# Performance work log

Hardware: AMD Instinct MI355X
Metric: run time of the kernel (lower is better)

## Reference

```python
import jax, jax.numpy as jnp
import numpy as np

B, S, DIM = 2, 1024, 1024
N_EXPERTS, K = 8, 2
VOCAB = 16384
HIDDEN = DIM * 8 // 3          # 2730
UP_OUT = HIDDEN * 2            # 5460 (swiglu doubling)


def setup_inputs() -> dict:
    key = jax.random.key(0)
    ks = jax.random.split(key, 5)
    x = jax.random.normal(ks[0], (B, S, DIM), dtype=jnp.float32)
    w_router = jax.random.normal(ks[1], (N_EXPERTS, DIM), dtype=jnp.float32) * 0.02
    w_up = jax.random.normal(ks[2], (N_EXPERTS, UP_OUT, DIM), dtype=jnp.float32) * 0.02
    w_down = jax.random.normal(ks[3], (N_EXPERTS, DIM, HIDDEN), dtype=jnp.float32) * 0.02
    w_proj = jax.random.normal(ks[4], (N_EXPERTS, VOCAB, DIM), dtype=jnp.float32) * 0.02
    return {"x": x, "w_router": w_router, "w_up": w_up, "w_down": w_down, "w_proj": w_proj}


def _grouped_linear(x_sorted, weight, group_sizes):
    # weight: [n_experts, out, in] (torch Linear layout) -> ragged_dot wants [g, in, out]
    return jax.lax.ragged_dot(x_sorted, jnp.swapaxes(weight, 1, 2), group_sizes)


def reference(x, w_router, w_up, w_down, w_proj):
    b, s, d = x.shape
    # Router (eval path): plain top-k of linear scores
    scores = jnp.einsum("bsd,nd->bsn", x, w_router)
    c, ids = jax.lax.top_k(scores, K)                   # [B,S,K]
    # Dispatch: replicate tokens k times, sort by expert id (stable, matching torch.sort)
    xe = jnp.broadcast_to(x[..., None, :], (b, s, K, d)).reshape(-1, d)   # [T, d]
    ids_flat = ids.reshape(-1)
    order = jnp.argsort(ids_flat)                        # stable sort indices
    x_sorted = xe[order]
    group_sizes = jnp.bincount(ids_flat, length=N_EXPERTS).astype(jnp.int32)
    # Expert swiglu MLP with residual (grouped GEMMs)
    skip = x_sorted
    h = _grouped_linear(x_sorted, w_up, group_sizes)     # [T, 2*HIDDEN]
    h_lin, h_gate = jnp.split(h, 2, axis=-1)
    h = h_lin * jax.nn.silu(h_gate)
    h = _grouped_linear(h, w_down, group_sizes) + skip   # [T, d]
    logits = _grouped_linear(h, w_proj, group_sizes)     # [T, VOCAB]
    # Postprocess: scatter back to original token order
    out = jnp.zeros_like(logits).at[order].set(logits)
    out = out.reshape(b, s, K, VOCAB)
    # Weighted top-k combine
    w = jax.nn.softmax(c, axis=-1)                       # [B,S,K]
    return jnp.sum(out * w[..., None], axis=-2)          # [B,S,VOCAB]
```

## Files before the change

kernel.cpp:

```cpp
#include <hip/hip_runtime.h>
#include <hip/hip_bf16.h>

typedef __bf16 bf16_t;
typedef __bf16 bf16x2 __attribute__((ext_vector_type(2)));
typedef __bf16 bf16x4 __attribute__((ext_vector_type(4)));
typedef __bf16 bf16x8 __attribute__((ext_vector_type(8)));
typedef float f32x4 __attribute__((ext_vector_type(4)));

#define DIM     1024
#define NEXP    8
#define VOCAB   16384
#define HIDDEN  2730
#define UPOUT   5460
#define NTOK    2048
#define NSLOT   4096
#define HRAW_LD 5472
#define H1_LD   2752
#define BM      256
#define MAXTILES 24

#define WS_COUNTS      0
#define WS_NTILES      64
#define WS_TILE_E      128
#define WS_TILE_M0     256
#define WS_TILE_MEND   384
#define WS_SLOT_IDS    1024
#define WS_SLOT_W      20480
#define WS_SLOT_OF_POS 40960
#define WS_POS_OF_SLOT 61440
#define WS_XSORTED     131072
#define WS_H2          8519680
#define WS_H1          16908288
#define WS_HRAW        39452672
#define WS_LOGITS      16908288ull
#define WS_NEED_BIG    (WS_LOGITS + (size_t)NSLOT * VOCAB * 2)

__device__ __forceinline__ void gload_lds16(const void* g, void* l) {
    __builtin_amdgcn_global_load_lds((const __attribute__((address_space(1))) void*)g,
                                     (__attribute__((address_space(3))) void*)l, 16, 0, 0);
}
__device__ __forceinline__ int swzm(int r) { return (r ^ (r >> 2)) & 3; }

__global__ __launch_bounds__(256) void router_kernel(const float* __restrict__ x,
        const float* __restrict__ wr, int* __restrict__ slot_ids,
        float* __restrict__ slot_w, int* __restrict__ counts) {
    const int lane = threadIdx.x & 63;
    const int wave = threadIdx.x >> 6;
    const int token = blockIdx.x * 4 + wave;
    const float* xrow = x + (size_t)token * DIM;
    float acc[NEXP];
#pragma unroll
    for (int e = 0; e < NEXP; ++e) acc[e] = 0.f;
#pragma unroll
    for (int i = 0; i < DIM / 64; ++i) {
        const int k = i * 64 + lane;
        const float xv = xrow[k];
#pragma unroll
        for (int e = 0; e < NEXP; ++e) acc[e] += xv * wr[e * DIM + k];
    }
#pragma unroll
    for (int off = 32; off > 0; off >>= 1) {
#pragma unroll
        for (int e = 0; e < NEXP; ++e) acc[e] += __shfl_xor(acc[e], off);
    }
    if (lane == 0) {
        float c0 = -1e30f; int b0 = 0;
#pragma unroll
        for (int e = 0; e < NEXP; ++e) if (acc[e] > c0) { c0 = acc[e]; b0 = e; }
        float c1 = -1e30f; int b1 = 0;
#pragma unroll
        for (int e = 0; e < NEXP; ++e) if (e != b0 && acc[e] > c1) { c1 = acc[e]; b1 = e; }
        slot_ids[token * 2 + 0] = b0;
        slot_ids[token * 2 + 1] = b1;
        const float w0 = 1.f / (1.f + expf(c1 - c0));
        slot_w[token * 2 + 0] = w0;
        slot_w[token * 2 + 1] = 1.f - w0;
        atomicAdd(&counts[b0], 1);
        atomicAdd(&counts[b1], 1);
    }
}

__global__ __launch_bounds__(512) void sched_kernel(const int* __restrict__ counts,
        int* __restrict__ ntiles, int* __restrict__ tile_e, int* __restrict__ tile_m0,
        int* __restrict__ tile_mend, const int* __restrict__ slot_ids,
        int* __restrict__ slot_of_pos, int* __restrict__ pos_of_slot) {
    __shared__ int offs[NEXP];
    if (threadIdx.x == 0) {
        int o = 0, nt = 0;
        for (int e = 0; e < NEXP; ++e) {
            offs[e] = o;
            const int c = counts[e];
            for (int m = 0; m < c; m += BM) {
                tile_e[nt] = e; tile_m0[nt] = o + m; tile_mend[nt] = o + c; ++nt;
            }
            o += c;
        }
        *ntiles = nt;
    }
    __syncthreads();
    const int e = threadIdx.x >> 6;
    const int lane = threadIdx.x & 63;
    int base = offs[e];
    for (int ch = 0; ch < NSLOT / 64; ++ch) {
        const int i = ch * 64 + lane;
        const int id = slot_ids[i];
        const unsigned long long m = __ballot(id == e);
        if (id == e) {
            const int rank = __popcll(m & ((1ull << lane) - 1ull));
            slot_of_pos[base + rank] = i;
            pos_of_slot[i] = base + rank;
        }
        base += __popcll(m);
    }
}

__global__ __launch_bounds__(256) void gather_kernel(const float* __restrict__ x,
        const int* __restrict__ slot_of_pos, bf16_t* __restrict__ xs) {
    const int row = blockIdx.x;
    const int t = threadIdx.x;
    const int tok = slot_of_pos[row] >> 1;
    const float4 v = *(const float4*)(x + (size_t)tok * DIM + t * 4);
    bf16x4 o;
    o.x = (bf16_t)v.x; o.y = (bf16_t)v.y; o.z = (bf16_t)v.z; o.w = (bf16_t)v.w;
    *(bf16x4*)(xs + (size_t)row * DIM + t * 4) = o;
}

__global__ __launch_bounds__(256) void swiglu_kernel(const bf16_t* __restrict__ hraw,
        bf16_t* __restrict__ h1) {
    const int row = blockIdx.x;
    const int col = blockIdx.y * 256 + threadIdx.x;
    if (col >= H1_LD) return;
    float o = 0.f;
    if (col < HIDDEN) {
        const float a = (float)hraw[(size_t)row * HRAW_LD + col];
        const float g = (float)hraw[(size_t)row * HRAW_LD + col + HIDDEN];
        o = a * (g / (1.f + expf(-g)));
    }
    h1[(size_t)row * H1_LD + col] = (bf16_t)o;
}

__global__ __launch_bounds__(256) void combine_kernel(const bf16_t* __restrict__ logits,
        const int* __restrict__ pos_of_slot, const float* __restrict__ slot_w,
        float* __restrict__ out) {
    const int t = blockIdx.x;
    const int v0 = (blockIdx.y * 256 + threadIdx.x) * 8;
    const int p0 = pos_of_slot[2 * t], p1 = pos_of_slot[2 * t + 1];
    const float w0 = slot_w[2 * t], w1 = slot_w[2 * t + 1];
    const bf16x8 a = *(const bf16x8*)(logits + (size_t)p0 * VOCAB + v0);
    const bf16x8 b = *(const bf16x8*)(logits + (size_t)p1 * VOCAB + v0);
    float o[8];
#pragma unroll
    for (int i = 0; i < 8; ++i) o[i] = w0 * (float)a[i] + w1 * (float)b[i];
    *(float4*)(out + (size_t)t * VOCAB + v0)     = make_float4(o[0], o[1], o[2], o[3]);
    *(float4*)(out + (size_t)t * VOCAB + v0 + 4) = make_float4(o[4], o[5], o[6], o[7]);
}

template <int EPI, bool SWZ>
__global__ __launch_bounds__(512, 2) void gemm_hi(
        const bf16_t* __restrict__ A,
        const float* __restrict__ B, int N,
        bf16_t* __restrict__ C, int ldc,
        const int* __restrict__ slot_of_pos,
        const float* __restrict__ slot_w,
        float* __restrict__ outp,
        const int* __restrict__ tile_e,
        const int* __restrict__ tile_m0,
        const int* __restrict__ tile_mend,
        const int* __restrict__ ntiles) {
    if (blockIdx.y >= (unsigned)*ntiles) return;
    constexpr int K = 1024, KT = 32;
    int bx = blockIdx.x;
    if constexpr (SWZ) bx = (bx & 7) * (gridDim.x >> 3) + (bx >> 3);
    const int e = tile_e[blockIdx.y];
    const int m0 = tile_m0[blockIdx.y];
    const int mend = tile_mend[blockIdx.y];
    const int n0 = bx * 256;
    const float* __restrict__ Bexp = B + (size_t)e * N * K;

    __shared__ bf16_t sA[2][256][32];
    __shared__ bf16_t sB[2][256][32];

    const int tid = threadIdx.x;
    const int lane = tid & 63;
    const int wave = tid >> 6;
    const int wr = wave >> 2;
    const int wc = wave & 3;
    const int fr = lane & 15;
    const int fq = lane >> 4;

    const int brow = tid >> 1;
    const int bseg = tid & 1;
    const float* bsrc = Bexp + (size_t)min(n0 + brow, N - 1) * K + bseg * 16;

    f32x4 acc[8][4] = {};

    auto stageA = [&](int buf, int kt) {
        const int k0 = min(kt, KT - 1) * 32;
#pragma unroll
        for (int j = 0; j < 2; ++j) {
            const int rb = wave * 32 + j * 16;
            const int r = rb + (lane >> 2);
            const int gr = min(m0 + r, NSLOT - 1);
            const int c16 = (lane & 3) ^ swzm(r);
            gload_lds16(A + (size_t)gr * K + k0 + c16 * 8, &sA[buf][rb][0]);
        }
    };
    auto loadB = [&](int kt, f32x4* v) {
        const int k0 = min(kt, KT - 1) * 32;
#pragma unroll
        for (int j = 0; j < 4; ++j) v[j] = *(const f32x4*)(bsrc + k0 + j * 4);
    };
    auto writeB = [&](int buf, const f32x4* v) {
#pragma unroll
        for (int u = 0; u < 2; ++u) {
            bf16x8 t;
            t[0] = (bf16_t)v[2*u][0]; t[1] = (bf16_t)v[2*u][1];
            t[2] = (bf16_t)v[2*u][2]; t[3] = (bf16_t)v[2*u][3];
            t[4] = (bf16_t)v[2*u+1][0]; t[5] = (bf16_t)v[2*u+1][1];
            t[6] = (bf16_t)v[2*u+1][2]; t[7] = (bf16_t)v[2*u+1][3];
            const int unit = (bseg * 2 + u) ^ swzm(brow);
            *(bf16x8*)&sB[buf][brow][unit * 8] = t;
        }
    };
    auto compute = [&](int buf) {
        bf16x8 bb[4];
#pragma unroll
        for (int ni = 0; ni < 4; ++ni) {
            const int r = wc * 64 + ni * 16 + fr;
            bb[ni] = *(const bf16x8*)&sB[buf][r][(fq ^ swzm(r)) * 8];
        }
        __builtin_amdgcn_s_setprio(1);
#pragma unroll
        for (int mi = 0; mi < 8; ++mi) {
            const int r = wr * 128 + mi * 16 + fr;
            const bf16x8 af = *(const bf16x8*)&sA[buf][r][(fq ^ swzm(r)) * 8];
#pragma unroll
            for (int ni = 0; ni < 4; ++ni)
                acc[mi][ni] = __builtin_amdgcn_mfma_f32_16x16x32_bf16(
                        af, bb[ni], acc[mi][ni], 0, 0, 0);
        }
        __builtin_amdgcn_s_setprio(0);
    };

    f32x4 P[4], Q[4];
    loadB(0, P);
    stageA(0, 0);
    loadB(1, Q);
    asm volatile("s_waitcnt vmcnt(6)" ::: "memory");
    writeB(0, P);
    asm volatile("s_waitcnt lgkmcnt(0)" ::: "memory");
    stageA(1, 1);

    for (int kt = 0; kt < KT; kt += 2) {
        loadB(kt + 2, P);
        asm volatile("s_waitcnt vmcnt(6)" ::: "memory");
        __builtin_amdgcn_s_barrier();
        asm volatile("" ::: "memory");
        writeB(1, Q);
        compute(0);
        asm volatile("s_waitcnt lgkmcnt(0)" ::: "memory");
        __builtin_amdgcn_s_barrier();
        asm volatile("" ::: "memory");
        stageA(0, kt + 2);
        loadB(kt + 3, Q);
        asm volatile("s_waitcnt vmcnt(6)" ::: "memory");
        __builtin_amdgcn_s_barrier();
        asm volatile("" ::: "memory");
        writeB(0, P);
        compute(1);
        asm volatile("s_waitcnt lgkmcnt(0)" ::: "memory");
        __builtin_amdgcn_s_barrier();
        asm volatile("" ::: "memory");
        stageA(1, kt + 3);
    }

#pragma unroll
    for (int mi = 0; mi < 8; ++mi) {
#pragma unroll
        for (int reg = 0; reg < 4; ++reg) {
            const int r = m0 + wr * 128 + mi * 16 + fq * 4 + reg;
            if (r >= mend) continue;
            int tok = 0; float wgt = 0.f;
            if constexpr (EPI == 2) {
                const int slot = slot_of_pos[r];
                tok = slot >> 1;
                wgt = slot_w[slot];
            }
#pragma unroll
            for (int ni = 0; ni < 4; ++ni) {
                const int c = n0 + wc * 64 + ni * 16 + fr;
                if (c >= N) continue;
                float v = acc[mi][ni][reg];
                if constexpr (EPI == 0) {
                    C[(size_t)r * ldc + c] = (bf16_t)v;
                } else {
                    unsafeAtomicAdd(&outp[(size_t)tok * VOCAB + c], v * wgt);
                }
            }
        }
    }
}

template <int EPI, int BN, bool SWZ>
__global__ __launch_bounds__(1024, 4) void gemm_mid(
        const bf16_t* __restrict__ A, int lda,
        const float* __restrict__ B, int N, int K, int KT, long bLast,
        bf16_t* __restrict__ C, int ldc,
        const bf16_t* __restrict__ skip,
        const int* __restrict__ tile_e,
        const int* __restrict__ tile_m0,
        const int* __restrict__ tile_mend,
        const int* __restrict__ ntiles) {
    if (blockIdx.y >= (unsigned)*ntiles) return;
    int bx = blockIdx.x;
    if constexpr (SWZ) bx = (bx & 7) * (gridDim.x >> 3) + (bx >> 3);
    const int e = tile_e[blockIdx.y];
    const int m0 = tile_m0[blockIdx.y];
    const int mend = tile_mend[blockIdx.y];
    const int n0 = bx * BN;

    constexpr int NI = BN / 64;

    __shared__ bf16_t sA[2][BM][32];
    __shared__ bf16_t sB[2][BN][32];

    const int tid = threadIdx.x;
    const int lane = tid & 63;
    const int wave = tid >> 6;
    const int wr = wave >> 2;
    const int wc = wave & 3;
    const int fr = lane & 15;
    const int fq = lane >> 4;

    f32x4 acc[4][NI] = {};

    auto stageA = [&](int buf, int kt) {
        const int k0 = min(kt, KT - 1) * 32;
        const int rb = wave * 16;
        const int r = rb + (lane >> 2);
        const int gr = min(m0 + r, NSLOT - 1);
        const int c16 = (lane & 3) ^ swzm(r);
        gload_lds16(A + (size_t)gr * lda + k0 + c16 * 8, &sA[buf][rb][0]);
    };
    auto loadB = [&](int kt, float2& vc) {
        const int k0 = min(kt, KT - 1) * 32;
        long fl = (long)e * N * K + (long)(n0 + wave * 4 + (lane >> 4)) * K
                  + k0 + (lane & 15) * 2;
        if (fl > bLast) fl = bLast;
        vc = *(const float2*)(B + fl);
    };
    auto writeB = [&](int buf, const float2& vc) {
        const int r = wave * 4 + (lane >> 4);
        bf16x2 t; t.x = (bf16_t)vc.x; t.y = (bf16_t)vc.y;
        const int q = lane & 15;
        char* p = (char*)&sB[buf][r][0] + (((q >> 2) ^ swzm(r)) * 16) + (q & 3) * 4;
        *(bf16x2*)p = t;
    };
    auto compute = [&](int buf) {
        bf16x8 af[4], bb[NI];
#pragma unroll
        for (int mi = 0; mi < 4; ++mi) {
            const int r = wr * 64 + mi * 16 + fr;
            af[mi] = *(const bf16x8*)&sA[buf][r][(fq ^ swzm(r)) * 8];
        }
#pragma unroll
        for (int ni = 0; ni < NI; ++ni) {
            const int r = wc * (BN / 4) + ni * 16 + fr;
            bb[ni] = *(const bf16x8*)&sB[buf][r][(fq ^ swzm(r)) * 8];
        }
        __builtin_amdgcn_s_setprio(1);
#pragma unroll
        for (int ni = 0; ni < NI; ++ni)
#pragma unroll
            for (int mi = 0; mi < 4; ++mi)
                acc[mi][ni] = __builtin_amdgcn_mfma_f32_16x16x32_bf16(
                        af[mi], bb[ni], acc[mi][ni], 0, 0, 0);
        __builtin_amdgcn_s_setprio(0);
    };

    float2 Pc, Qc;
    loadB(0, Pc);
    stageA(0, 0);
    loadB(1, Qc);
    asm volatile("s_waitcnt vmcnt(2)" ::: "memory");
    writeB(0, Pc);
    asm volatile("s_waitcnt lgkmcnt(0)" ::: "memory");
    stageA(1, 1);

    for (int kt = 0; kt < KT; kt += 2) {
        loadB(kt + 2, Pc);
        asm volatile("s_waitcnt vmcnt(2)" ::: "memory");
        __builtin_amdgcn_s_barrier();
        asm volatile("" ::: "memory");
        writeB(1, Qc);
        compute(0);
        asm volatile("s_waitcnt lgkmcnt(0)" ::: "memory");
        __builtin_amdgcn_s_barrier();
        asm volatile("" ::: "memory");
        stageA(0, kt + 2);
        loadB(kt + 3, Qc);
        asm volatile("s_waitcnt vmcnt(2)" ::: "memory");
        __builtin_amdgcn_s_barrier();
        asm volatile("" ::: "memory");
        writeB(0, Pc);
        compute(1);
        asm volatile("s_waitcnt lgkmcnt(0)" ::: "memory");
        __builtin_amdgcn_s_barrier();
        asm volatile("" ::: "memory");
        stageA(1, kt + 3);
    }

#pragma unroll
    for (int mi = 0; mi < 4; ++mi) {
#pragma unroll
        for (int reg = 0; reg < 4; ++reg) {
            const int r = m0 + wr * 64 + mi * 16 + fq * 4 + reg;
            if (r >= mend) continue;
#pragma unroll
            for (int ni = 0; ni < NI; ++ni) {
                const int c = n0 + wc * (BN / 4) + ni * 16 + fr;
                if (c >= N) continue;
                float v = acc[mi][ni][reg];
                if constexpr (EPI == 1) v += (float)skip[(size_t)r * DIM + c];
                C[(size_t)r * ldc + c] = (bf16_t)v;
            }
        }
    }
}

extern "C" void kernel_launch(void* const* d_in, const int* in_sizes, int n_in,
                              void* d_out, int out_size, void* d_ws, size_t ws_size,
                              hipStream_t stream) {
    const float* x        = (const float*)d_in[0];
    const float* w_router = (const float*)d_in[1];
    const float* w_up     = (const float*)d_in[2];
    const float* w_down   = (const float*)d_in[3];
    const float* w_proj   = (const float*)d_in[4];
    float* out = (float*)d_out;
    char* ws = (char*)d_ws;

    int*    counts      = (int*)(ws + WS_COUNTS);
    int*    ntiles      = (int*)(ws + WS_NTILES);
    int*    tile_e      = (int*)(ws + WS_TILE_E);
    int*    tile_m0     = (int*)(ws + WS_TILE_M0);
    int*    tile_mend   = (int*)(ws + WS_TILE_MEND);
    int*    slot_ids    = (int*)(ws + WS_SLOT_IDS);
    float*  slot_w      = (float*)(ws + WS_SLOT_W);
    int*    slot_of_pos = (int*)(ws + WS_SLOT_OF_POS);
    int*    pos_of_slot = (int*)(ws + WS_POS_OF_SLOT);
    bf16_t* x_sorted    = (bf16_t*)(ws + WS_XSORTED);
    bf16_t* h2          = (bf16_t*)(ws + WS_H2);
    bf16_t* h1          = (bf16_t*)(ws + WS_H1);
    bf16_t* h_raw       = (bf16_t*)(ws + WS_HRAW);
    bf16_t* logits      = (bf16_t*)(ws + WS_LOGITS);

    const bool bigws = ws_size >= WS_NEED_BIG;

    hipMemsetAsync(d_ws, 0, 1024, stream);

    router_kernel<<<NTOK / 4, 256, 0, stream>>>(x, w_router, slot_ids, slot_w, counts);
    sched_kernel<<<1, 512, 0, stream>>>(counts, ntiles, tile_e, tile_m0, tile_mend,
                                        slot_ids, slot_of_pos, pos_of_slot);
    gather_kernel<<<NSLOT, 256, 0, stream>>>(x, slot_of_pos, x_sorted);

    gemm_hi<0, false><<<dim3((UPOUT + 255) / 256, MAXTILES), 512, 0, stream>>>(
        x_sorted, w_up, UPOUT, h_raw, HRAW_LD,
        nullptr, nullptr, nullptr, tile_e, tile_m0, tile_mend, ntiles);

    swiglu_kernel<<<dim3(NSLOT, (H1_LD + 255) / 256), 256, 0, stream>>>(h_raw, h1);

    gemm_mid<1, 64, true><<<dim3(DIM / 64, MAXTILES), 1024, 0, stream>>>(
        h1, H1_LD, w_down, DIM, HIDDEN, (HIDDEN + 31) / 32,
        (long)NEXP * DIM * HIDDEN - 2,
        h2, DIM, x_sorted, tile_e, tile_m0, tile_mend, ntiles);

    if (bigws) {
        gemm_hi<0, true><<<dim3(VOCAB / 256, MAXTILES), 512, 0, stream>>>(
            h2, w_proj, VOCAB, logits, VOCAB,
            nullptr, nullptr, nullptr, tile_e, tile_m0, tile_mend, ntiles);
        combine_kernel<<<dim3(NTOK, VOCAB / (256 * 8)), 256, 0, stream>>>(
            logits, pos_of_slot, slot_w, out);
    } else {
        hipMemsetAsync(d_out, 0, (size_t)out_size * sizeof(float), stream);
        gemm_hi<2, true><<<dim3(VOCAB / 256, MAXTILES), 512, 0, stream>>>(
            h2, w_proj, VOCAB, nullptr, 0,
            slot_of_pos, slot_w, out, tile_e, tile_m0, tile_mend, ntiles);
    }
}
```

Measured before the change: 706.2 us.

## Use 1024-thread blocks with packed 128x64 LDS layout in big GEMM

Doubles the GEMM block to 1024 threads (16 waves) on the same 256x256 tile, so each wave holds a 64x64 accumulator instead of 128x64. This halves per-thread registers. The shared-memory tiles are repacked from [256][32] into [128][64] with an XOR swizzle, and each thread now loads one A and one B chunk per K-step. The aim is more resident waves to hide latency, at the cost of more barrier participants and a lower MFMA-to-LDS-read ratio per wave.

```diff
diff --git a/kernel.cpp b/kernel.cpp
--- a/kernel.cpp
+++ b/kernel.cpp
@@ -156,7 +156,7 @@
 }
 
 template <int EPI, bool SWZ>
-__global__ __launch_bounds__(512, 2) void gemm_hi(
+__global__ __launch_bounds__(1024, 4) void gemm_pk(
         const bf16_t* __restrict__ A,
         const float* __restrict__ B, int N,
         bf16_t* __restrict__ C, int ldc,
@@ -177,8 +177,8 @@
     const int n0 = bx * 256;
     const float* __restrict__ Bexp = B + (size_t)e * N * K;
 
-    __shared__ bf16_t sA[2][256][32];
-    __shared__ bf16_t sB[2][256][32];
+    __shared__ bf16_t sA[2][128][64];
+    __shared__ bf16_t sB[2][128][64];
 
     const int tid = threadIdx.x;
     const int lane = tid & 63;
@@ -188,52 +188,53 @@
     const int fr = lane & 15;
     const int fq = lane >> 4;
 
-    const int brow = tid >> 1;
-    const int bseg = tid & 1;
-    const float* bsrc = Bexp + (size_t)min(n0 + brow, N - 1) * K + bseg * 16;
-
-    f32x4 acc[8][4] = {};
+    const int a_ou = (lane & 7) ^ (lane >> 3);
+    const int a_r  = wave * 8 + (lane >> 3) + ((a_ou & 4) << 5);
+    const int a_k16 = (a_ou & 3) * 8;
+
+    const int bp  = tid >> 3;
+    const int bu  = tid & 7;
+    const int bou = bu ^ (bp & 7);
+    const int b_row = bp + ((bou & 4) << 5);
+    const int b_k   = (bou & 3) * 8;
+    const float* bsrc = Bexp + (size_t)min(n0 + b_row, N - 1) * K + b_k;
+
+    f32x4 acc[4][4] = {};
 
     auto stageA = [&](int buf, int kt) {
         const int k0 = min(kt, KT - 1) * 32;
-#pragma unroll
-        for (int j = 0; j < 2; ++j) {
-            const int rb = wave * 32 + j * 16;
-            const int r = rb + (lane >> 2);
-            const int gr = min(m0 + r, NSLOT - 1);
-            const int c16 = (lane & 3) ^ swzm(r);
-            gload_lds16(A + (size_t)gr * K + k0 + c16 * 8, &sA[buf][rb][0]);
-        }
-    };
-    auto loadB = [&](int kt, f32x4* v) {
+        const int gr = min(m0 + a_r, NSLOT - 1);
+        gload_lds16(A + (size_t)gr * K + k0 + a_k16, &sA[buf][wave * 8][0]);
+    };
+    auto loadB = [&](int kt, f32x4& v0, f32x4& v1) {
         const int k0 = min(kt, KT - 1) * 32;
-#pragma unroll
-        for (int j = 0; j < 4; ++j) v[j] = *(const f32x4*)(bsrc + k0 + j * 4);
-    };
-    auto writeB = [&](int buf, const f32x4* v) {
-#pragma unroll
-        for (int u = 0; u < 2; ++u) {
-            bf16x8 t;
-            t[0] = (bf16_t)v[2*u][0]; t[1] = (bf16_t)v[2*u][1];
-            t[2] = (bf16_t)v[2*u][2]; t[3] = (bf16_t)v[2*u][3];
-            t[4] = (bf16_t)v[2*u+1][0]; t[5] = (bf16_t)v[2*u+1][1];
-            t[6] = (bf16_t)v[2*u+1][2]; t[7] = (bf16_t)v[2*u+1][3];
-            const int unit = (bseg * 2 + u) ^ swzm(brow);
-            *(bf16x8*)&sB[buf][brow][unit * 8] = t;
-        }
+        v0 = *(const f32x4*)(bsrc + k0);
+        v1 = *(const f32x4*)(bsrc + k0 + 4);
+    };
+    auto writeB = [&](int buf, const f32x4& v0, const f32x4& v1) {
+        bf16x8 t;
+        t[0] = (bf16_t)v0[0]; t[1] = (bf16_t)v0[1];
+        t[2] = (bf16_t)v0[2]; t[3] = (bf16_t)v0[3];
+        t[4] = (bf16_t)v1[0]; t[5] = (bf16_t)v1[1];
+        t[6] = (bf16_t)v1[2]; t[7] = (bf16_t)v1[3];
+        *(bf16x8*)&sB[buf][bp][bu * 8] = t;
     };
     auto compute = [&](int buf) {
         bf16x8 bb[4];
 #pragma unroll
         for (int ni = 0; ni < 4; ++ni) {
             const int r = wc * 64 + ni * 16 + fr;
-            bb[ni] = *(const bf16x8*)&sB[buf][r][(fq ^ swzm(r)) * 8];
+            const int p = r & 127;
+            const int u = (((r >> 7) << 2) + fq) ^ (fr & 7);
+            bb[ni] = *(const bf16x8*)&sB[buf][p][u * 8];
         }
         __builtin_amdgcn_s_setprio(1);
 #pragma unroll
-        for (int mi = 0; mi < 8; ++mi) {
-            const int r = wr * 128 + mi * 16 + fr;
-            const bf16x8 af = *(const bf16x8*)&sA[buf][r][(fq ^ swzm(r)) * 8];
+        for (int mi = 0; mi < 4; ++mi) {
+            const int r = wr * 64 + mi * 16 + fr;
+            const int p = r & 127;
+            const int u = (((r >> 7) << 2) + fq) ^ (fr & 7);
+            const bf16x8 af = *(const bf16x8*)&sA[buf][p][u * 8];
 #pragma unroll
             for (int ni = 0; ni < 4; ++ni)
                 acc[mi][ni] = __builtin_amdgcn_mfma_f32_16x16x32_bf16(
@@ -242,31 +243,31 @@
         __builtin_amdgcn_s_setprio(0);
     };
 
-    f32x4 P[4], Q[4];
-    loadB(0, P);
+    f32x4 P0, P1, Q0, Q1;
+    loadB(0, P0, P1);
     stageA(0, 0);
-    loadB(1, Q);
-    asm volatile("s_waitcnt vmcnt(6)" ::: "memory");
-    writeB(0, P);
+    loadB(1, Q0, Q1);
+    asm volatile("s_waitcnt vmcnt(3)" ::: "memory");
+    writeB(0, P0, P1);
     asm volatile("s_waitcnt lgkmcnt(0)" ::: "memory");
     stageA(1, 1);
 
     for (int kt = 0; kt < KT; kt += 2) {
-        loadB(kt + 2, P);
-        asm volatile("s_waitcnt vmcnt(6)" ::: "memory");
-        __builtin_amdgcn_s_barrier();
-        asm volatile("" ::: "memory");
-        writeB(1, Q);
+        loadB(kt + 2, P0, P1);
+        asm volatile("s_waitcnt vmcnt(3)" ::: "memory");
+        __builtin_amdgcn_s_barrier();
+        asm volatile("" ::: "memory");
+        writeB(1, Q0, Q1);
         compute(0);
         asm volatile("s_waitcnt lgkmcnt(0)" ::: "memory");
         __builtin_amdgcn_s_barrier();
         asm volatile("" ::: "memory");
         stageA(0, kt + 2);
-        loadB(kt + 3, Q);
-        asm volatile("s_waitcnt vmcnt(6)" ::: "memory");
-        __builtin_amdgcn_s_barrier();
-        asm volatile("" ::: "memory");
-        writeB(0, P);
+        loadB(kt + 3, Q0, Q1);
+        asm volatile("s_waitcnt vmcnt(3)" ::: "memory");
+        __builtin_amdgcn_s_barrier();
+        asm volatile("" ::: "memory");
+        writeB(0, P0, P1);
         compute(1);
         asm volatile("s_waitcnt lgkmcnt(0)" ::: "memory");
         __builtin_amdgcn_s_barrier();
@@ -275,10 +276,10 @@
     }
 
 #pragma unroll
-    for (int mi = 0; mi < 8; ++mi) {
+    for (int mi = 0; mi < 4; ++mi) {
 #pragma unroll
         for (int reg = 0; reg < 4; ++reg) {
-            const int r = m0 + wr * 128 + mi * 16 + fq * 4 + reg;
+            const int r = m0 + wr * 64 + mi * 16 + fq * 4 + reg;
             if (r >= mend) continue;
             int tok = 0; float wgt = 0.f;
             if constexpr (EPI == 2) {
@@ -463,7 +464,7 @@
                                         slot_ids, slot_of_pos, pos_of_slot);
     gather_kernel<<<NSLOT, 256, 0, stream>>>(x, slot_of_pos, x_sorted);
 
-    gemm_hi<0, false><<<dim3((UPOUT + 255) / 256, MAXTILES), 512, 0, stream>>>(
+    gemm_pk<0, false><<<dim3((UPOUT + 255) / 256, MAXTILES), 1024, 0, stream>>>(
         x_sorted, w_up, UPOUT, h_raw, HRAW_LD,
         nullptr, nullptr, nullptr, tile_e, tile_m0, tile_mend, ntiles);
 
@@ -475,14 +476,14 @@
         h2, DIM, x_sorted, tile_e, tile_m0, tile_mend, ntiles);
 
     if (bigws) {
-        gemm_hi<0, true><<<dim3(VOCAB / 256, MAXTILES), 512, 0, stream>>>(
+        gemm_pk<0, true><<<dim3(VOCAB / 256, MAXTILES), 1024, 0, stream>>>(
             h2, w_proj, VOCAB, logits, VOCAB,
             nullptr, nullptr, nullptr, tile_e, tile_m0, tile_mend, ntiles);
         combine_kernel<<<dim3(NTOK, VOCAB / (256 * 8)), 256, 0, stream>>>(
             logits, pos_of_slot, slot_w, out);
     } else {
         hipMemsetAsync(d_out, 0, (size_t)out_size * sizeof(float), stream);
-        gemm_hi<2, true><<<dim3(VOCAB / 256, MAXTILES), 512, 0, stream>>>(
+        gemm_pk<2, true><<<dim3(VOCAB / 256, MAXTILES), 1024, 0, stream>>>(
             h2, w_proj, VOCAB, nullptr, 0,
             slot_of_pos, slot_w, out, tile_e, tile_m0, tile_mend, ntiles);
     }
```

After: 648.3 us. 8.2% less time.

## Double waves per block in expert GEMM with coalesced B loads and deeper prefetch

Applied to the files above, without the earlier changes.

Replaces the 512-thread grouped GEMM with a 1024-thread variant. Each wave now computes a 64x64 sub-tile instead of 128x64 of the same 256x256 block tile. The fp32 weight tile is loaded with a lane-contiguous coalesced pattern, and the register prefetch is deepened to three k-steps ahead using a rotated four-buffer scheme. The aim is more latency hiding and better global-load efficiency for the weight stream. In exchange it adds barrier contention across 16 waves, and the aggressive launch bound may force register spilling.

```diff
diff --git a/kernel.cpp b/kernel.cpp
--- a/kernel.cpp
+++ b/kernel.cpp
@@ -156,7 +156,7 @@
 }
 
 template <int EPI, bool SWZ>
-__global__ __launch_bounds__(512, 2) void gemm_hi(
+__global__ __launch_bounds__(1024, 4) void gemm_d2(
         const bf16_t* __restrict__ A,
         const float* __restrict__ B, int N,
         bf16_t* __restrict__ C, int ldc,
@@ -188,38 +188,34 @@
     const int fr = lane & 15;
     const int fq = lane >> 4;
 
-    const int brow = tid >> 1;
-    const int bseg = tid & 1;
-    const float* bsrc = Bexp + (size_t)min(n0 + brow, N - 1) * K + bseg * 16;
-
-    f32x4 acc[8][4] = {};
+    f32x4 acc[4][4] = {};
 
     auto stageA = [&](int buf, int kt) {
         const int k0 = min(kt, KT - 1) * 32;
-#pragma unroll
-        for (int j = 0; j < 2; ++j) {
-            const int rb = wave * 32 + j * 16;
-            const int r = rb + (lane >> 2);
-            const int gr = min(m0 + r, NSLOT - 1);
-            const int c16 = (lane & 3) ^ swzm(r);
-            gload_lds16(A + (size_t)gr * K + k0 + c16 * 8, &sA[buf][rb][0]);
-        }
-    };
-    auto loadB = [&](int kt, f32x4* v) {
+        const int rb = wave * 16;
+        const int r = rb + (lane >> 2);
+        const int gr = min(m0 + r, NSLOT - 1);
+        const int c16 = (lane & 3) ^ swzm(r);
+        gload_lds16(A + (size_t)gr * K + k0 + c16 * 8, &sA[buf][rb][0]);
+    };
+    auto loadB = [&](int kt, f32x4* va) {
         const int k0 = min(kt, KT - 1) * 32;
 #pragma unroll
-        for (int j = 0; j < 4; ++j) v[j] = *(const f32x4*)(bsrc + k0 + j * 4);
-    };
-    auto writeB = [&](int buf, const f32x4* v) {
-#pragma unroll
-        for (int u = 0; u < 2; ++u) {
-            bf16x8 t;
-            t[0] = (bf16_t)v[2*u][0]; t[1] = (bf16_t)v[2*u][1];
-            t[2] = (bf16_t)v[2*u][2]; t[3] = (bf16_t)v[2*u][3];
-            t[4] = (bf16_t)v[2*u+1][0]; t[5] = (bf16_t)v[2*u+1][1];
-            t[6] = (bf16_t)v[2*u+1][2]; t[7] = (bf16_t)v[2*u+1][3];
-            const int unit = (bseg * 2 + u) ^ swzm(brow);
-            *(bf16x8*)&sB[buf][brow][unit * 8] = t;
+        for (int nb = 0; nb < 2; ++nb) {
+            const int gr = min(n0 + nb * 128 + wave * 8 + (lane >> 3), N - 1);
+            va[nb] = *(const f32x4*)(Bexp + (size_t)gr * K + k0 + (lane & 7) * 4);
+        }
+    };
+    auto writeB = [&](int buf, const f32x4* va) {
+#pragma unroll
+        for (int nb = 0; nb < 2; ++nb) {
+            const int r = nb * 128 + wave * 8 + (lane >> 3);
+            bf16x4 t;
+            t.x = (bf16_t)va[nb].x; t.y = (bf16_t)va[nb].y;
+            t.z = (bf16_t)va[nb].z; t.w = (bf16_t)va[nb].w;
+            char* p = (char*)&sB[buf][r][0]
+                    + ((((lane & 7) >> 1) ^ swzm(r)) * 16) + (lane & 1) * 8;
+            *(bf16x4*)p = t;
         }
     };
     auto compute = [&](int buf) {
@@ -231,8 +227,8 @@
         }
         __builtin_amdgcn_s_setprio(1);
 #pragma unroll
-        for (int mi = 0; mi < 8; ++mi) {
-            const int r = wr * 128 + mi * 16 + fr;
+        for (int mi = 0; mi < 4; ++mi) {
+            const int r = wr * 64 + mi * 16 + fr;
             const bf16x8 af = *(const bf16x8*)&sA[buf][r][(fq ^ swzm(r)) * 8];
 #pragma unroll
             for (int ni = 0; ni < 4; ++ni)
@@ -242,43 +238,42 @@
         __builtin_amdgcn_s_setprio(0);
     };
 
-    f32x4 P[4], Q[4];
-    loadB(0, P);
+    f32x4 S0[2], S1[2], S2[2], S3[2];
+
+    loadB(0, S0);
+    loadB(1, S1);
     stageA(0, 0);
-    loadB(1, Q);
-    asm volatile("s_waitcnt vmcnt(6)" ::: "memory");
-    writeB(0, P);
+    loadB(2, S2);
+    asm volatile("s_waitcnt vmcnt(5)" ::: "memory");
+    writeB(0, S0);
     asm volatile("s_waitcnt lgkmcnt(0)" ::: "memory");
     stageA(1, 1);
 
-    for (int kt = 0; kt < KT; kt += 2) {
-        loadB(kt + 2, P);
-        asm volatile("s_waitcnt vmcnt(6)" ::: "memory");
-        __builtin_amdgcn_s_barrier();
-        asm volatile("" ::: "memory");
-        writeB(1, Q);
-        compute(0);
-        asm volatile("s_waitcnt lgkmcnt(0)" ::: "memory");
-        __builtin_amdgcn_s_barrier();
-        asm volatile("" ::: "memory");
-        stageA(0, kt + 2);
-        loadB(kt + 3, Q);
-        asm volatile("s_waitcnt vmcnt(6)" ::: "memory");
-        __builtin_amdgcn_s_barrier();
-        asm volatile("" ::: "memory");
-        writeB(0, P);
-        compute(1);
-        asm volatile("s_waitcnt lgkmcnt(0)" ::: "memory");
-        __builtin_amdgcn_s_barrier();
-        asm volatile("" ::: "memory");
-        stageA(1, kt + 3);
-    }
-
-#pragma unroll
-    for (int mi = 0; mi < 8; ++mi) {
+#define D2_STEP(T, SL, SW)                                          \
+    loadB((T) + 3, SL);                                             \
+    asm volatile("s_waitcnt vmcnt(5)" ::: "memory");                \
+    __builtin_amdgcn_s_barrier();                                   \
+    asm volatile("" ::: "memory");                                  \
+    writeB(((T) + 1) & 1, SW);                                      \
+    compute((T) & 1);                                               \
+    asm volatile("s_waitcnt lgkmcnt(0)" ::: "memory");              \
+    __builtin_amdgcn_s_barrier();                                   \
+    asm volatile("" ::: "memory");                                  \
+    stageA((T) & 1, (T) + 2);
+
+    for (int kt = 0; kt < KT; kt += 4) {
+        D2_STEP(kt + 0, S3, S1);
+        D2_STEP(kt + 1, S0, S2);
+        D2_STEP(kt + 2, S1, S3);
+        D2_STEP(kt + 3, S2, S0);
+    }
+#undef D2_STEP
+
+#pragma unroll
+    for (int mi = 0; mi < 4; ++mi) {
 #pragma unroll
         for (int reg = 0; reg < 4; ++reg) {
-            const int r = m0 + wr * 128 + mi * 16 + fq * 4 + reg;
+            const int r = m0 + wr * 64 + mi * 16 + fq * 4 + reg;
             if (r >= mend) continue;
             int tok = 0; float wgt = 0.f;
             if constexpr (EPI == 2) {
@@ -463,7 +458,7 @@
                                         slot_ids, slot_of_pos, pos_of_slot);
     gather_kernel<<<NSLOT, 256, 0, stream>>>(x, slot_of_pos, x_sorted);
 
-    gemm_hi<0, false><<<dim3((UPOUT + 255) / 256, MAXTILES), 512, 0, stream>>>(
+    gemm_d2<0, false><<<dim3((UPOUT + 255) / 256, MAXTILES), 1024, 0, stream>>>(
         x_sorted, w_up, UPOUT, h_raw, HRAW_LD,
         nullptr, nullptr, nullptr, tile_e, tile_m0, tile_mend, ntiles);
 
@@ -475,14 +470,14 @@
         h2, DIM, x_sorted, tile_e, tile_m0, tile_mend, ntiles);
 
     if (bigws) {
-        gemm_hi<0, true><<<dim3(VOCAB / 256, MAXTILES), 512, 0, stream>>>(
+        gemm_d2<0, true><<<dim3(VOCAB / 256, MAXTILES), 1024, 0, stream>>>(
             h2, w_proj, VOCAB, logits, VOCAB,
             nullptr, nullptr, nullptr, tile_e, tile_m0, tile_mend, ntiles);
         combine_kernel<<<dim3(NTOK, VOCAB / (256 * 8)), 256, 0, stream>>>(
             logits, pos_of_slot, slot_w, out);
     } else {
         hipMemsetAsync(d_out, 0, (size_t)out_size * sizeof(float), stream);
-        gemm_hi<2, true><<<dim3(VOCAB / 256, MAXTILES), 512, 0, stream>>>(
+        gemm_d2<2, true><<<dim3(VOCAB / 256, MAXTILES), 1024, 0, stream>>>(
             h2, w_proj, VOCAB, nullptr, 0,
             slot_of_pos, slot_w, out, tile_e, tile_m0, tile_mend, ntiles);
     }
```

Result: faster. 642.3 us (-9.0%).
